# Kernel optimization log

Measured on AMD Instinct MI355X. Metric: run time of the kernel, lower is better.

Reference implementation:

```python
import jax, jax.numpy as jnp
import numpy as np

N_HEAD = 16
HEAD_DIM = 64
EPS_RMS = 1e-6


def _rope(x, cos, sin):
    # x: [B, T, H, D]; cos/sin: [T, D//2] broadcast to [1, T, 1, D//2]
    d2 = x.shape[-1] // 2
    x1, x2 = x[..., :d2], x[..., d2:]
    c = cos[None, :, None, :]
    s = sin[None, :, None, :]
    return jnp.concatenate([x1 * c + x2 * s, -x1 * s + x2 * c], axis=-1)


def _rms_norm(x):
    return x * jax.lax.rsqrt(jnp.mean(x * x, axis=-1, keepdims=True) + EPS_RMS)


def setup_inputs() -> dict:
    key = jax.random.key(0)
    ks = jax.random.split(key, 7)
    B, T, C = 1, 4096, 1024
    x = jax.random.normal(ks[0], (B, T, C), dtype=jnp.float32)
    # realistic rotary angles
    d2 = HEAD_DIM // 2
    inv_freq = 1.0 / (10000.0 ** (np.arange(0, d2, dtype=np.float32) / d2))
    ang = np.arange(T, dtype=np.float32)[:, None] * inv_freq[None, :]
    cos = jnp.asarray(np.cos(ang), dtype=jnp.float32)
    sin = jnp.asarray(np.sin(ang), dtype=jnp.float32)
    scale = 0.02
    wq = jax.random.normal(ks[1], (C, C), dtype=jnp.float32) * scale
    wk = jax.random.normal(ks[2], (C, C), dtype=jnp.float32) * scale
    wv = jax.random.normal(ks[3], (C, C), dtype=jnp.float32) * scale
    wproj = jax.random.normal(ks[4], (C, C), dtype=jnp.float32) * scale
    return {"x": x, "cos": cos, "sin": sin, "wq": wq, "wk": wk, "wv": wv, "wproj": wproj}


def reference(x, cos, sin, wq, wk, wv, wproj):
    B, T, C = x.shape
    H, D = N_HEAD, HEAD_DIM
    # QKV projections (torch Linear: x @ W.T)
    q = (x @ wq.T).reshape(B, T, H, D)
    k = (x @ wk.T).reshape(B, T, H, D)
    v = (x @ wv.T).reshape(B, T, H, D)
    # RoPE then QK RMS-norm
    q = _rms_norm(_rope(q, cos, sin))
    k = _rms_norm(_rope(k, cos, sin))
    # [B, H, T, D]
    q = q.transpose(0, 2, 1, 3)
    k = k.transpose(0, 2, 1, 3)
    v = v.transpose(0, 2, 1, 3)
    scores = jnp.einsum('bhqd,bhkd->bhqk', q, k) * (1.0 / D ** 0.5)
    # causal mask (kv_cache is None, Tq == Tk == T)
    mask = jnp.tril(jnp.ones((T, T), dtype=bool))
    scores = jnp.where(mask[None, None, :, :], scores, -jnp.inf)
    attn = jax.nn.sigmoid(scores)  # sigmoid(-inf) == 0
    y = jnp.einsum('bhqk,bhkd->bhqd', attn, v)
    y = y / (T ** 0.5 + 1e-6)
    y = y.transpose(0, 2, 1, 3).reshape(B, T, C)
    return y @ wproj.T
```

## Files before the change

kernel.cpp:

```cpp
#include <hip/hip_runtime.h>

typedef __attribute__((ext_vector_type(8))) short bf16x8;
typedef __attribute__((ext_vector_type(4))) float f32x4;
typedef __attribute__((ext_vector_type(16))) float f32x16;

__device__ inline f32x4 mfma16(bf16x8 a, bf16x8 b, f32x4 c) {
    return __builtin_amdgcn_mfma_f32_16x16x32_bf16(a, b, c, 0, 0, 0);
}
__device__ inline f32x16 mfma32(bf16x8 a, bf16x8 b, f32x16 c) {
    return __builtin_amdgcn_mfma_f32_32x32x16_bf16(a, b, c, 0, 0, 0);
}

__device__ inline short f2bf(float f) {
    unsigned u = __builtin_bit_cast(unsigned, f);
    unsigned r = (u + 0x7fffu + ((u >> 16) & 1u)) >> 16;
    return (short)r;
}
__device__ inline float bf2f(short h) {
    unsigned u = ((unsigned)(unsigned short)h) << 16;
    return __builtin_bit_cast(float, u);
}

__device__ inline unsigned cvt_pk_bf16(float lo, float hi) {
    unsigned r;
    asm("v_cvt_pk_bf16_f32 %0, %1, %2" : "=v"(r) : "v"(lo), "v"(hi));
    return r;
}
__device__ inline void plane_swap(unsigned& a, unsigned& b) {
    asm("v_permlane32_swap_b32 %0, %1" : "+v"(a), "+v"(b));
}
__device__ inline float exp2_hw(float x) {
    float r;
    asm("v_exp_f32 %0, %1" : "=v"(r) : "v"(x));
    return r;
}

#define GAS(p) (const __attribute__((address_space(1))) void*)(p)
#define LAS(p) (__attribute__((address_space(3))) void*)(p)

#define T_SEQ 4096
#define C_DIM 1024
#define N_HEAD 16
#define HEAD_DIM 64
#define QSCALE (-0.18033688011112042f)

__global__ __launch_bounds__(256) void cast5(
    const float* __restrict__ s0, const float* __restrict__ s1,
    const float* __restrict__ s2, const float* __restrict__ s3,
    const float* __restrict__ s4,
    short* __restrict__ d0, short* __restrict__ d1, short* __restrict__ d2,
    short* __restrict__ d3, short* __restrict__ d4,
    int n0, int n1, int n2, int n3, int n4)
{
    int z = blockIdx.y;
    const float* s; short* d; int n;
    switch (z) {
        case 0: s = s0; d = d0; n = n0; break;
        case 1: s = s1; d = d1; n = n1; break;
        case 2: s = s2; d = d2; n = n2; break;
        case 3: s = s3; d = d3; n = n3; break;
        default: s = s4; d = d4; n = n4; break;
    }
    int i = (blockIdx.x * 256 + threadIdx.x) * 4;
    if (i >= n) return;
    float4 v = *(const float4*)&s[i];
    short4 o;
    o.x = f2bf(v.x); o.y = f2bf(v.y); o.z = f2bf(v.z); o.w = f2bf(v.w);
    *(short4*)&d[i] = o;
}

#define QSTAGE(t_, b_) do {                                                      \
    int k0_ = (t_) * 32;                                                         \
    _Pragma("unroll")                                                            \
    for (int s2_ = 0; s2_ < 2; s2_++) {                                          \
        int rbase_ = wave * 32 + s2_ * 16;                                       \
        __builtin_amdgcn_global_load_lds(                                        \
            GAS(&A[(size_t)(row0 + rbase_ + srow) * KK + k0_ + scol]),           \
            LAS(&sA[b_][rbase_ * 32]), 16, 0, 0);                                \
        __builtin_amdgcn_global_load_lds(                                        \
            GAS(&B[(size_t)(col0 + rbase_ + srow) * KK + k0_ + scol]),           \
            LAS(&sB[b_][rbase_ * 32]), 16, 0, 0);                                \
    }                                                                            \
} while (0)

__global__ __launch_bounds__(256) void gemm_qkv(
    const short* __restrict__ A,
    const short* __restrict__ B0, const short* __restrict__ B1,
    const short* __restrict__ B2,
    short* __restrict__ qnb, short* __restrict__ knb, short* __restrict__ vnb,
    const float* __restrict__ cosT, const float* __restrict__ sinT)
{
    int z = blockIdx.z;
    const short* B = (z == 0) ? B0 : ((z == 1) ? B1 : B2);
    short* dst     = (z == 0) ? qnb : ((z == 1) ? knb : vnb);

    __shared__ alignas(16) short sA[2][128 * 32];
    __shared__ alignas(16) short sB[2][128 * 32];

    int tid  = threadIdx.x;
    int wave = tid >> 6, lane = tid & 63;
    int lhi  = lane >> 4, llo = lane & 15;
    int wr   = wave >> 1, wc = wave & 1;
    int row0 = blockIdx.x * 128, col0 = blockIdx.y * 128;
    const int KK = C_DIM;

    int srow = lane >> 2;
    int scol = (lane & 3) * 8;

    f32x4 acc[4][4];
#pragma unroll
    for (int m = 0; m < 4; m++)
#pragma unroll
        for (int n = 0; n < 4; n++)
            acc[m][n] = (f32x4){0.f, 0.f, 0.f, 0.f};

    QSTAGE(0, 0);
    asm volatile("s_waitcnt vmcnt(0)" ::: "memory");
    __builtin_amdgcn_s_barrier();
    int bufg = 0;
    for (int t = 0; t < 32; t++) {
        if (t + 1 < 32) QSTAGE(t + 1, bufg ^ 1);

        bf16x8 af[4], bfv[4];
#pragma unroll
        for (int m = 0; m < 4; m++)
            af[m] = *(const bf16x8*)&sA[bufg][(wr * 64 + m * 16 + llo) * 32 + lhi * 8];
#pragma unroll
        for (int n = 0; n < 4; n++)
            bfv[n] = *(const bf16x8*)&sB[bufg][(wc * 64 + n * 16 + llo) * 32 + lhi * 8];
        __builtin_amdgcn_s_setprio(1);
#pragma unroll
        for (int m = 0; m < 4; m++)
#pragma unroll
            for (int n = 0; n < 4; n++)
                acc[m][n] = mfma16(af[m], bfv[n], acc[m][n]);
        __builtin_amdgcn_s_setprio(0);

        asm volatile("s_waitcnt vmcnt(0)" ::: "memory");
        __builtin_amdgcn_s_barrier();
        bufg ^= 1;
    }

    int hH = blockIdx.y * 2 + wc;
    if (z < 2) {
        float osc = z ? 1.0f : QSCALE;
#pragma unroll
        for (int m = 0; m < 4; m++)
#pragma unroll
            for (int r = 0; r < 4; r++) {
                int row = row0 + wr * 64 + m * 16 + lhi * 4 + r;
                float c0 = cosT[row * 32 + llo],      c1 = cosT[row * 32 + 16 + llo];
                float s0 = sinT[row * 32 + llo],      s1 = sinT[row * 32 + 16 + llo];
                float e0 = acc[m][0][r], e1 = acc[m][1][r];
                float e2 = acc[m][2][r], e3 = acc[m][3][r];
                float r0 = e0 * c0 + e2 * s0;
                float r1 = e1 * c1 + e3 * s1;
                float r2 = e2 * c0 - e0 * s0;
                float r3 = e3 * c1 - e1 * s1;
                float sq = r0 * r0 + r1 * r1 + r2 * r2 + r3 * r3;
                sq += __shfl_xor(sq, 1);
                sq += __shfl_xor(sq, 2);
                sq += __shfl_xor(sq, 4);
                sq += __shfl_xor(sq, 8);
                float inv = rsqrtf(sq * (1.0f / 64.0f) + 1e-6f) * osc;
                size_t base = ((size_t)hH * T_SEQ + row) * HEAD_DIM + llo;
                dst[base +  0] = f2bf(r0 * inv);
                dst[base + 16] = f2bf(r1 * inv);
                dst[base + 32] = f2bf(r2 * inv);
                dst[base + 48] = f2bf(r3 * inv);
            }
    } else {
#pragma unroll
        for (int m = 0; m < 4; m++)
#pragma unroll
            for (int r = 0; r < 4; r++) {
                int row = row0 + wr * 64 + m * 16 + lhi * 4 + r;
                size_t base = ((size_t)hH * T_SEQ + row) * HEAD_DIM + llo;
#pragma unroll
                for (int n = 0; n < 4; n++)
                    dst[base + n * 16] = f2bf(acc[m][n][r]);
            }
    }
}

__global__ __launch_bounds__(256) void gemm_proj(
    const short* __restrict__ A, const short* __restrict__ B,
    float* __restrict__ C, int M, int N, int K)
{
    __shared__ alignas(16) short sA[2][128 * 32];
    __shared__ alignas(16) short sB[2][128 * 32];

    int tid  = threadIdx.x;
    int wave = tid >> 6, lane = tid & 63;
    int lhi  = lane >> 4, llo = lane & 15;
    int wr   = wave >> 1, wc = wave & 1;
    int row0 = blockIdx.x * 128, col0 = blockIdx.y * 128;
    const int KK = K;

    int srow = lane >> 2;
    int scol = (lane & 3) * 8;

    f32x4 acc[4][4];
#pragma unroll
    for (int m = 0; m < 4; m++)
#pragma unroll
        for (int n = 0; n < 4; n++)
            acc[m][n] = (f32x4){0.f, 0.f, 0.f, 0.f};

    int nt = K >> 5;
    QSTAGE(0, 0);
    asm volatile("s_waitcnt vmcnt(0)" ::: "memory");
    __builtin_amdgcn_s_barrier();
    int bufg = 0;
    for (int t = 0; t < nt; t++) {
        if (t + 1 < nt) QSTAGE(t + 1, bufg ^ 1);

        bf16x8 af[4], bfv[4];
#pragma unroll
        for (int m = 0; m < 4; m++)
            af[m] = *(const bf16x8*)&sA[bufg][(wr * 64 + m * 16 + llo) * 32 + lhi * 8];
#pragma unroll
        for (int n = 0; n < 4; n++)
            bfv[n] = *(const bf16x8*)&sB[bufg][(wc * 64 + n * 16 + llo) * 32 + lhi * 8];
        __builtin_amdgcn_s_setprio(1);
#pragma unroll
        for (int m = 0; m < 4; m++)
#pragma unroll
            for (int n = 0; n < 4; n++)
                acc[m][n] = mfma16(af[m], bfv[n], acc[m][n]);
        __builtin_amdgcn_s_setprio(0);

        asm volatile("s_waitcnt vmcnt(0)" ::: "memory");
        __builtin_amdgcn_s_barrier();
        bufg ^= 1;
    }

#pragma unroll
    for (int m = 0; m < 4; m++)
#pragma unroll
        for (int n = 0; n < 4; n++)
#pragma unroll
            for (int r = 0; r < 4; r++) {
                int row = row0 + wr * 64 + m * 16 + lhi * 4 + r;
                int col = col0 + wc * 64 + n * 16 + llo;
                C[(size_t)row * N + col] = acc[m][n][r];
            }
}

__global__ __launch_bounds__(256) void vtrans(
    const short* __restrict__ vnb, short* __restrict__ vt)
{
    __shared__ short sT[64 * 65];
    int h = blockIdx.y, tb = blockIdx.x;
    int tid = threadIdx.x;
    const float inv64 = 1.0f / (64.0f + 1e-6f);
#pragma unroll
    for (int i = 0; i < 16; i++) {
        int linear = i * 256 + tid;
        int r = linear >> 6, c = linear & 63;
        float v = bf2f(vnb[((size_t)h * T_SEQ + tb * 64 + r) * HEAD_DIM + c]) * inv64;
        sT[c * 65 + r] = f2bf(v);
    }
    __syncthreads();
#pragma unroll
    for (int i = 0; i < 16; i++) {
        int linear = i * 256 + tid;
        int dd = linear >> 6, tt = linear & 63;
        vt[((size_t)(h * HEAD_DIM + dd)) * T_SEQ + tb * 64 + tt] = sT[dd * 65 + tt];
    }
}


#define STAGE6(s_, bf_) do {                                                     \
    int kb_ = (s_) * 64;                                                         \
    int r_  = lane >> 3;                                                         \
    int ss_ = (lane & 7) ^ r_;                                                   \
    __builtin_amdgcn_global_load_lds(                                            \
        GAS(Kh + (size_t)(kb_ + wv * 16 + r_) * HEAD_DIM + ss_ * 8),             \
        LAS(Smem + (bf_) * 8192 + (wv * 16) * 128), 16, 0, 0);                   \
    __builtin_amdgcn_global_load_lds(                                            \
        GAS(Kh + (size_t)(kb_ + wv * 16 + 8 + r_) * HEAD_DIM + ss_ * 8),         \
        LAS(Smem + (bf_) * 8192 + (wv * 16 + 8) * 128), 16, 0, 0);               \
    __builtin_amdgcn_global_load_lds(                                            \
        GAS(Vh + (size_t)(wv * 16 + r_) * T_SEQ + kb_ + ss_ * 8),                \
        LAS(Smem + 16384 + (bf_) * 8192 + (wv * 16) * 128), 16, 0, 0);           \
    __builtin_amdgcn_global_load_lds(                                            \
        GAS(Vh + (size_t)(wv * 16 + 8 + r_) * T_SEQ + kb_ + ss_ * 8),            \
        LAS(Smem + 16384 + (bf_) * 8192 + (wv * 16 + 8) * 128), 16, 0, 0);       \
} while (0)

__global__ __launch_bounds__(256, 4) void attn10(
    const short* __restrict__ qn, const short* __restrict__ kn,
    const short* __restrict__ vt, short* __restrict__ yb)
{
    __shared__ alignas(16) char Smem[32768];

    int id = blockIdx.x;
    int h  = id & 15;
    int pp = id >> 4;

    int tid = threadIdx.x, wv = tid >> 6, lane = tid & 63;
    int lo = lane & 31, hi = lane >> 5;
    int band = wv & 1, tm = wv >> 1;

    const short* Qh = qn + (size_t)h * T_SEQ * HEAD_DIM;
    const short* Kh = kn + (size_t)h * T_SEQ * HEAD_DIM;
    const short* Vh = vt + (size_t)h * HEAD_DIM * T_SEQ;

    unsigned sw   = (unsigned)((lo & 7) << 4);
    unsigned krow = (unsigned)((tm * 32 + lo) * 128);
    unsigned ko0 = krow + ((0u * 32 + hi * 16) ^ sw);
    unsigned ko1 = krow + ((1u * 32 + hi * 16) ^ sw);
    unsigned ko2 = krow + ((2u * 32 + hi * 16) ^ sw);
    unsigned ko3 = krow + ((3u * 32 + hi * 16) ^ sw);
    unsigned vrow0 = (unsigned)(lo * 128)        + 16384u;
    unsigned vrow1 = (unsigned)((32 + lo) * 128) + 16384u;
    unsigned vo00 = vrow0 + (((unsigned)(tm * 64 + 0 * 32 + hi * 16)) ^ sw);
    unsigned vo01 = vrow0 + (((unsigned)(tm * 64 + 1 * 32 + hi * 16)) ^ sw);
    unsigned vo10 = vrow1 + (((unsigned)(tm * 64 + 0 * 32 + hi * 16)) ^ sw);
    unsigned vo11 = vrow1 + (((unsigned)(tm * 64 + 1 * 32 + hi * 16)) ^ sw);

    f32x16 zed;
#pragma unroll
    for (int r = 0; r < 16; r++) zed[r] = 0.f;

    for (int hf = 0; hf < 2; hf++) {
        int t  = hf ? pp : (63 - pp);
        int ns = t + 1;

        int q0 = t * 64;
        int qrow  = q0 + band * 32 + lo;
        int qmaxw = q0 + band * 32 + 31;

        const short* Qr = &Qh[(size_t)qrow * HEAD_DIM + hi * 8];
        bf16x8 qf0 = *(const bf16x8*)&Qr[0];
        bf16x8 qf1 = *(const bf16x8*)&Qr[16];
        bf16x8 qf2 = *(const bf16x8*)&Qr[32];
        bf16x8 qf3 = *(const bf16x8*)&Qr[48];

        f32x16 yac0, yac1;
#pragma unroll
        for (int r = 0; r < 16; r++) { yac0[r] = 0.f; yac1[r] = 0.f; }

        STAGE6(0, 0);
        int buf = 0;
        for (int s = 0; s < ns; s++) {
            if (s + 1 < ns) {
                STAGE6(s + 1, buf ^ 1);
                asm volatile("s_waitcnt vmcnt(4)" ::: "memory");
            } else {
                asm volatile("s_waitcnt vmcnt(0)" ::: "memory");
            }
            __builtin_amdgcn_s_barrier();

            int kb0 = s * 64 + tm * 32;
            if (kb0 <= qmaxw) {
                const char* B_ = Smem + (buf << 13);
                bf16x8 kf0 = *(const bf16x8*)(B_ + ko0);
                bf16x8 kf1 = *(const bf16x8*)(B_ + ko1);
                bf16x8 kf2 = *(const bf16x8*)(B_ + ko2);
                bf16x8 kf3 = *(const bf16x8*)(B_ + ko3);
                bf16x8 vf00 = *(const bf16x8*)(B_ + vo00);
                bf16x8 vf01 = *(const bf16x8*)(B_ + vo01);
                bf16x8 vf10 = *(const bf16x8*)(B_ + vo10);
                bf16x8 vf11 = *(const bf16x8*)(B_ + vo11);

                f32x16 sv;
                __builtin_amdgcn_s_setprio(1);
                sv = mfma32(kf0, qf0, zed);
                sv = mfma32(kf1, qf1, sv);
                sv = mfma32(kf2, qf2, sv);
                sv = mfma32(kf3, qf3, sv);
                __builtin_amdgcn_s_setprio(0);

                if (kb0 + 31 > q0 + band * 32) {
#pragma unroll
                    for (int r = 0; r < 16; r++) {
                        int kvg = kb0 + (r & 3) + 8 * (r >> 2) + 4 * hi;
                        float pv = __builtin_amdgcn_rcpf(1.f + exp2_hw(sv[r]));
                        sv[r] = (kvg <= qrow) ? pv : 0.f;
                    }
                } else {
#pragma unroll
                    for (int r = 0; r < 16; r++)
                        sv[r] = __builtin_amdgcn_rcpf(1.f + exp2_hw(sv[r]));
                }

#pragma unroll
                for (int k2 = 0; k2 < 2; k2++) {
                    unsigned wA = cvt_pk_bf16(sv[8 * k2 + 0], sv[8 * k2 + 1]);
                    unsigned wC = cvt_pk_bf16(sv[8 * k2 + 2], sv[8 * k2 + 3]);
                    unsigned wB = cvt_pk_bf16(sv[8 * k2 + 4], sv[8 * k2 + 5]);
                    unsigned wD = cvt_pk_bf16(sv[8 * k2 + 6], sv[8 * k2 + 7]);
                    plane_swap(wA, wB);
                    plane_swap(wC, wD);
                    union { unsigned u[4]; bf16x8 v; } pw;
                    pw.u[0] = wA; pw.u[1] = wC; pw.u[2] = wB; pw.u[3] = wD;
                    __builtin_amdgcn_s_setprio(1);
                    yac0 = mfma32(pw.v, k2 ? vf01 : vf00, yac0);
                    yac1 = mfma32(pw.v, k2 ? vf11 : vf10, yac1);
                    __builtin_amdgcn_s_setprio(0);
                }
            }
            asm volatile("" ::: "memory");
            __builtin_amdgcn_s_barrier();
            buf ^= 1;
        }

        __syncthreads();
        float* Yred = (float*)Smem;
        if (tm == 1) {
#pragma unroll
            for (int d = 0; d < 2; d++)
#pragma unroll
                for (int r = 0; r < 16; r++) {
                    int crow = (r & 3) + 8 * (r >> 2) + 4 * hi;
                    Yred[(band * 32 + crow) * 64 + d * 32 + lo] = d ? yac1[r] : yac0[r];
                }
        }
        __syncthreads();
        if (tm == 0) {
#pragma unroll
            for (int d = 0; d < 2; d++)
#pragma unroll
                for (int r = 0; r < 16; r++) {
                    int crow = (r & 3) + 8 * (r >> 2) + 4 * hi;
                    float v = (d ? yac1[r] : yac0[r]) + Yred[(band * 32 + crow) * 64 + d * 32 + lo];
                    yb[(size_t)(q0 + band * 32 + crow) * C_DIM + h * HEAD_DIM + d * 32 + lo] = f2bf(v);
                }
        }
        __syncthreads();
    }
}

extern "C" void kernel_launch(void* const* d_in, const int* in_sizes, int n_in,
                              void* d_out, int out_size, void* d_ws, size_t ws_size,
                              hipStream_t stream)
{
    const float* x    = (const float*)d_in[0];
    const float* cosT = (const float*)d_in[1];
    const float* sinT = (const float*)d_in[2];
    const float* wq   = (const float*)d_in[3];
    const float* wk   = (const float*)d_in[4];
    const float* wv   = (const float*)d_in[5];
    const float* wp   = (const float*)d_in[6];

    char* ws = (char*)d_ws;
    const size_t MB = 1024 * 1024;
    short* xb    = (short*)(ws + 0);
    short* wqb   = (short*)(ws + 8  * MB);
    short* wkb   = (short*)(ws + 10 * MB);
    short* wvb   = (short*)(ws + 12 * MB);
    short* wpb   = (short*)(ws + 14 * MB);
    short* qnb   = (short*)(ws + 16 * MB);
    short* knb   = (short*)(ws + 24 * MB);
    short* vnb   = (short*)(ws + 32 * MB);
    short* vtb   = (short*)(ws + 40 * MB);
    short* yb    = (short*)(ws + 48 * MB);

    cast5<<<dim3(4096, 5, 1), 256, 0, stream>>>(
        x, wq, wk, wv, wp, xb, wqb, wkb, wvb, wpb,
        T_SEQ * C_DIM, C_DIM * C_DIM, C_DIM * C_DIM, C_DIM * C_DIM, C_DIM * C_DIM);

    gemm_qkv<<<dim3(32, 8, 3), 256, 0, stream>>>(
        xb, wqb, wkb, wvb, qnb, knb, vnb, cosT, sinT);

    vtrans<<<dim3(64, 16, 1), 256, 0, stream>>>(vnb, vtb);

    attn10<<<512, 256, 0, stream>>>(qnb, knb, vtb, yb);

    gemm_proj<<<dim3(32, 8, 1), 256, 0, stream>>>(
        yb, wpb, (float*)d_out, T_SEQ, C_DIM, C_DIM);
}
```

Baseline: 159.6 us.

## Split attention into one tile per block, fold V scale into proj weights, vectorize vtrans

The attention kernel now gives each block a single 64-row query tile, launching 1024 blocks instead of 512 blocks that each handled a long and a short tile. The block-to-tile map interleaves long and short tiles so the causal work stays balanced across the dispatch. The 1/(64+eps) output scale moves from the V transpose into the bf16 cast of the projection weight. vtrans switches to 16-byte vector loads and stores with a padded LDS tile. Folding the scale into the weights changes bf16 rounding slightly, and more blocks add per-block Q-load and reduction overhead.

```diff
diff --git a/kernel.cpp b/kernel.cpp
--- a/kernel.cpp
+++ b/kernel.cpp
@@ -43,6 +43,7 @@
 #define N_HEAD 16
 #define HEAD_DIM 64
 #define QSCALE (-0.18033688011112042f)
+#define INV64 (1.0f / (64.0f + 1e-6f))
 
 __global__ __launch_bounds__(256) void cast5(
     const float* __restrict__ s0, const float* __restrict__ s1,
@@ -61,11 +62,13 @@
         case 3: s = s3; d = d3; n = n3; break;
         default: s = s4; d = d4; n = n4; break;
     }
+    float sc = (z == 4) ? INV64 : 1.0f;
     int i = (blockIdx.x * 256 + threadIdx.x) * 4;
     if (i >= n) return;
     float4 v = *(const float4*)&s[i];
     short4 o;
-    o.x = f2bf(v.x); o.y = f2bf(v.y); o.z = f2bf(v.z); o.w = f2bf(v.w);
+    o.x = f2bf(v.x * sc); o.y = f2bf(v.y * sc);
+    o.z = f2bf(v.z * sc); o.w = f2bf(v.w * sc);
     *(short4*)&d[i] = o;
 }
 
@@ -250,23 +253,24 @@
 __global__ __launch_bounds__(256) void vtrans(
     const short* __restrict__ vnb, short* __restrict__ vt)
 {
-    __shared__ short sT[64 * 65];
+    __shared__ short sT[64 * 72];
     int h = blockIdx.y, tb = blockIdx.x;
     int tid = threadIdx.x;
-    const float inv64 = 1.0f / (64.0f + 1e-6f);
-#pragma unroll
-    for (int i = 0; i < 16; i++) {
-        int linear = i * 256 + tid;
-        int r = linear >> 6, c = linear & 63;
-        float v = bf2f(vnb[((size_t)h * T_SEQ + tb * 64 + r) * HEAD_DIM + c]) * inv64;
-        sT[c * 65 + r] = f2bf(v);
+#pragma unroll
+    for (int p = 0; p < 2; p++) {
+        int r  = p * 32 + (tid >> 3);
+        int c0 = (tid & 7) * 8;
+        bf16x8 v = *(const bf16x8*)&vnb[((size_t)h * T_SEQ + tb * 64 + r) * HEAD_DIM + c0];
+#pragma unroll
+        for (int j = 0; j < 8; j++) sT[(c0 + j) * 72 + r] = v[j];
     }
     __syncthreads();
 #pragma unroll
-    for (int i = 0; i < 16; i++) {
-        int linear = i * 256 + tid;
-        int dd = linear >> 6, tt = linear & 63;
-        vt[((size_t)(h * HEAD_DIM + dd)) * T_SEQ + tb * 64 + tt] = sT[dd * 65 + tt];
+    for (int p = 0; p < 2; p++) {
+        int dd = p * 32 + (tid >> 3);
+        int t0 = (tid & 7) * 8;
+        bf16x8 o = *(const bf16x8*)&sT[dd * 72 + t0];
+        *(bf16x8*)&vt[((size_t)(h * HEAD_DIM + dd)) * T_SEQ + tb * 64 + t0] = o;
     }
 }
 
@@ -289,7 +293,7 @@
         LAS(Smem + 16384 + (bf_) * 8192 + (wv * 16 + 8) * 128), 16, 0, 0);       \
 } while (0)
 
-__global__ __launch_bounds__(256, 4) void attn10(
+__global__ __launch_bounds__(256, 4) void attn6(
     const short* __restrict__ qn, const short* __restrict__ kn,
     const short* __restrict__ vt, short* __restrict__ yb)
 {
@@ -297,7 +301,10 @@
 
     int id = blockIdx.x;
     int h  = id & 15;
-    int pp = id >> 4;
+    int g  = id >> 4;
+    int t  = (g < 16) ? (63 - g) : (g < 32) ? (g - 16)
+           : (g < 48) ? (79 - g) : (g - 32);
+    int ns = t + 1;
 
     int tid = threadIdx.x, wv = tid >> 6, lane = tid & 63;
     int lo = lane & 31, hi = lane >> 5;
@@ -306,6 +313,24 @@
     const short* Qh = qn + (size_t)h * T_SEQ * HEAD_DIM;
     const short* Kh = kn + (size_t)h * T_SEQ * HEAD_DIM;
     const short* Vh = vt + (size_t)h * HEAD_DIM * T_SEQ;
+
+    int q0 = t * 64;
+    int qrow  = q0 + band * 32 + lo;
+    int qmaxw = q0 + band * 32 + 31;
+
+    const short* Qr = &Qh[(size_t)qrow * HEAD_DIM + hi * 8];
+    bf16x8 qf0 = *(const bf16x8*)&Qr[0];
+    bf16x8 qf1 = *(const bf16x8*)&Qr[16];
+    bf16x8 qf2 = *(const bf16x8*)&Qr[32];
+    bf16x8 qf3 = *(const bf16x8*)&Qr[48];
+
+    f32x16 zed;
+#pragma unroll
+    for (int r = 0; r < 16; r++) zed[r] = 0.f;
+
+    f32x16 yac0, yac1;
+#pragma unroll
+    for (int r = 0; r < 16; r++) { yac0[r] = 0.f; yac1[r] = 0.f; }
 
     unsigned sw   = (unsigned)((lo & 7) << 4);
     unsigned krow = (unsigned)((tm * 32 + lo) * 128);
@@ -320,116 +345,92 @@
     unsigned vo10 = vrow1 + (((unsigned)(tm * 64 + 0 * 32 + hi * 16)) ^ sw);
     unsigned vo11 = vrow1 + (((unsigned)(tm * 64 + 1 * 32 + hi * 16)) ^ sw);
 
-    f32x16 zed;
-#pragma unroll
-    for (int r = 0; r < 16; r++) zed[r] = 0.f;
-
-    for (int hf = 0; hf < 2; hf++) {
-        int t  = hf ? pp : (63 - pp);
-        int ns = t + 1;
-
-        int q0 = t * 64;
-        int qrow  = q0 + band * 32 + lo;
-        int qmaxw = q0 + band * 32 + 31;
-
-        const short* Qr = &Qh[(size_t)qrow * HEAD_DIM + hi * 8];
-        bf16x8 qf0 = *(const bf16x8*)&Qr[0];
-        bf16x8 qf1 = *(const bf16x8*)&Qr[16];
-        bf16x8 qf2 = *(const bf16x8*)&Qr[32];
-        bf16x8 qf3 = *(const bf16x8*)&Qr[48];
-
-        f32x16 yac0, yac1;
-#pragma unroll
-        for (int r = 0; r < 16; r++) { yac0[r] = 0.f; yac1[r] = 0.f; }
-
-        STAGE6(0, 0);
-        int buf = 0;
-        for (int s = 0; s < ns; s++) {
-            if (s + 1 < ns) {
-                STAGE6(s + 1, buf ^ 1);
-                asm volatile("s_waitcnt vmcnt(4)" ::: "memory");
+    STAGE6(0, 0);
+    int buf = 0;
+    for (int s = 0; s < ns; s++) {
+        if (s + 1 < ns) {
+            STAGE6(s + 1, buf ^ 1);
+            asm volatile("s_waitcnt vmcnt(4)" ::: "memory");
+        } else {
+            asm volatile("s_waitcnt vmcnt(0)" ::: "memory");
+        }
+        __builtin_amdgcn_s_barrier();
+
+        int kb0 = s * 64 + tm * 32;
+        if (kb0 <= qmaxw) {
+            const char* B_ = Smem + (buf << 13);
+            bf16x8 kf0 = *(const bf16x8*)(B_ + ko0);
+            bf16x8 kf1 = *(const bf16x8*)(B_ + ko1);
+            bf16x8 kf2 = *(const bf16x8*)(B_ + ko2);
+            bf16x8 kf3 = *(const bf16x8*)(B_ + ko3);
+            bf16x8 vf00 = *(const bf16x8*)(B_ + vo00);
+            bf16x8 vf01 = *(const bf16x8*)(B_ + vo01);
+            bf16x8 vf10 = *(const bf16x8*)(B_ + vo10);
+            bf16x8 vf11 = *(const bf16x8*)(B_ + vo11);
+
+            f32x16 sv;
+            __builtin_amdgcn_s_setprio(1);
+            sv = mfma32(kf0, qf0, zed);
+            sv = mfma32(kf1, qf1, sv);
+            sv = mfma32(kf2, qf2, sv);
+            sv = mfma32(kf3, qf3, sv);
+            __builtin_amdgcn_s_setprio(0);
+
+            if (kb0 + 31 > q0 + band * 32) {
+#pragma unroll
+                for (int r = 0; r < 16; r++) {
+                    int kvg = kb0 + (r & 3) + 8 * (r >> 2) + 4 * hi;
+                    float pv = __builtin_amdgcn_rcpf(1.f + exp2_hw(sv[r]));
+                    sv[r] = (kvg <= qrow) ? pv : 0.f;
+                }
             } else {
-                asm volatile("s_waitcnt vmcnt(0)" ::: "memory");
-            }
-            __builtin_amdgcn_s_barrier();
-
-            int kb0 = s * 64 + tm * 32;
-            if (kb0 <= qmaxw) {
-                const char* B_ = Smem + (buf << 13);
-                bf16x8 kf0 = *(const bf16x8*)(B_ + ko0);
-                bf16x8 kf1 = *(const bf16x8*)(B_ + ko1);
-                bf16x8 kf2 = *(const bf16x8*)(B_ + ko2);
-                bf16x8 kf3 = *(const bf16x8*)(B_ + ko3);
-                bf16x8 vf00 = *(const bf16x8*)(B_ + vo00);
-                bf16x8 vf01 = *(const bf16x8*)(B_ + vo01);
-                bf16x8 vf10 = *(const bf16x8*)(B_ + vo10);
-                bf16x8 vf11 = *(const bf16x8*)(B_ + vo11);
-
-                f32x16 sv;
+#pragma unroll
+                for (int r = 0; r < 16; r++)
+                    sv[r] = __builtin_amdgcn_rcpf(1.f + exp2_hw(sv[r]));
+            }
+
+#pragma unroll
+            for (int k2 = 0; k2 < 2; k2++) {
+                unsigned wA = cvt_pk_bf16(sv[8 * k2 + 0], sv[8 * k2 + 1]);
+                unsigned wC = cvt_pk_bf16(sv[8 * k2 + 2], sv[8 * k2 + 3]);
+                unsigned wB = cvt_pk_bf16(sv[8 * k2 + 4], sv[8 * k2 + 5]);
+                unsigned wD = cvt_pk_bf16(sv[8 * k2 + 6], sv[8 * k2 + 7]);
+                plane_swap(wA, wB);
+                plane_swap(wC, wD);
+                union { unsigned u[4]; bf16x8 v; } pw;
+                pw.u[0] = wA; pw.u[1] = wC; pw.u[2] = wB; pw.u[3] = wD;
                 __builtin_amdgcn_s_setprio(1);
-                sv = mfma32(kf0, qf0, zed);
-                sv = mfma32(kf1, qf1, sv);
-                sv = mfma32(kf2, qf2, sv);
-                sv = mfma32(kf3, qf3, sv);
+                yac0 = mfma32(pw.v, k2 ? vf01 : vf00, yac0);
+                yac1 = mfma32(pw.v, k2 ? vf11 : vf10, yac1);
                 __builtin_amdgcn_s_setprio(0);
-
-                if (kb0 + 31 > q0 + band * 32) {
-#pragma unroll
-                    for (int r = 0; r < 16; r++) {
-                        int kvg = kb0 + (r & 3) + 8 * (r >> 2) + 4 * hi;
-                        float pv = __builtin_amdgcn_rcpf(1.f + exp2_hw(sv[r]));
-                        sv[r] = (kvg <= qrow) ? pv : 0.f;
-                    }
-                } else {
-#pragma unroll
-                    for (int r = 0; r < 16; r++)
-                        sv[r] = __builtin_amdgcn_rcpf(1.f + exp2_hw(sv[r]));
-                }
-
-#pragma unroll
-                for (int k2 = 0; k2 < 2; k2++) {
-                    unsigned wA = cvt_pk_bf16(sv[8 * k2 + 0], sv[8 * k2 + 1]);
-                    unsigned wC = cvt_pk_bf16(sv[8 * k2 + 2], sv[8 * k2 + 3]);
-                    unsigned wB = cvt_pk_bf16(sv[8 * k2 + 4], sv[8 * k2 + 5]);
-                    unsigned wD = cvt_pk_bf16(sv[8 * k2 + 6], sv[8 * k2 + 7]);
-                    plane_swap(wA, wB);
-                    plane_swap(wC, wD);
-                    union { unsigned u[4]; bf16x8 v; } pw;
-                    pw.u[0] = wA; pw.u[1] = wC; pw.u[2] = wB; pw.u[3] = wD;
-                    __builtin_amdgcn_s_setprio(1);
-                    yac0 = mfma32(pw.v, k2 ? vf01 : vf00, yac0);
-                    yac1 = mfma32(pw.v, k2 ? vf11 : vf10, yac1);
-                    __builtin_amdgcn_s_setprio(0);
-                }
-            }
-            asm volatile("" ::: "memory");
-            __builtin_amdgcn_s_barrier();
-            buf ^= 1;
+            }
         }
-
-        __syncthreads();
-        float* Yred = (float*)Smem;
-        if (tm == 1) {
-#pragma unroll
-            for (int d = 0; d < 2; d++)
-#pragma unroll
-                for (int r = 0; r < 16; r++) {
-                    int crow = (r & 3) + 8 * (r >> 2) + 4 * hi;
-                    Yred[(band * 32 + crow) * 64 + d * 32 + lo] = d ? yac1[r] : yac0[r];
-                }
-        }
-        __syncthreads();
-        if (tm == 0) {
-#pragma unroll
-            for (int d = 0; d < 2; d++)
-#pragma unroll
-                for (int r = 0; r < 16; r++) {
-                    int crow = (r & 3) + 8 * (r >> 2) + 4 * hi;
-                    float v = (d ? yac1[r] : yac0[r]) + Yred[(band * 32 + crow) * 64 + d * 32 + lo];
-                    yb[(size_t)(q0 + band * 32 + crow) * C_DIM + h * HEAD_DIM + d * 32 + lo] = f2bf(v);
-                }
-        }
-        __syncthreads();
+        asm volatile("" ::: "memory");
+        __builtin_amdgcn_s_barrier();
+        buf ^= 1;
+    }
+
+    __syncthreads();
+    float* Yred = (float*)Smem;
+    if (tm == 1) {
+#pragma unroll
+        for (int d = 0; d < 2; d++)
+#pragma unroll
+            for (int r = 0; r < 16; r++) {
+                int crow = (r & 3) + 8 * (r >> 2) + 4 * hi;
+                Yred[(band * 32 + crow) * 64 + d * 32 + lo] = d ? yac1[r] : yac0[r];
+            }
+    }
+    __syncthreads();
+    if (tm == 0) {
+#pragma unroll
+        for (int d = 0; d < 2; d++)
+#pragma unroll
+            for (int r = 0; r < 16; r++) {
+                int crow = (r & 3) + 8 * (r >> 2) + 4 * hi;
+                float v = (d ? yac1[r] : yac0[r]) + Yred[(band * 32 + crow) * 64 + d * 32 + lo];
+                yb[(size_t)(q0 + band * 32 + crow) * C_DIM + h * HEAD_DIM + d * 32 + lo] = f2bf(v);
+            }
     }
 }
 
@@ -467,7 +468,7 @@
 
     vtrans<<<dim3(64, 16, 1), 256, 0, stream>>>(vnb, vtb);
 
-    attn10<<<512, 256, 0, stream>>>(qnb, knb, vtb, yb);
+    attn6<<<1024, 256, 0, stream>>>(qnb, knb, vtb, yb);
 
     gemm_proj<<<dim3(32, 8, 1), 256, 0, stream>>>(
         yb, wpb, (float*)d_out, T_SEQ, C_DIM, C_DIM);
```

Measured after the change: 145.8 us. -8.7%, faster.
